# Performance work log

Hardware: AMD Instinct MI355X
Metric: run time of the kernel (lower is better)

Reference implementation:

```python
import jax, jax.numpy as jnp
import numpy as np
from jax.scipy.special import gammaln

N_TIMES = 131072
MAX_ITER = 4
DAMPING = 0.5
PREC_FLOOR = 1e-6
DEG = 20
TWO_PI = 2.0 * np.pi


def _gh_nodes(deg):
    # Nodes/weights such that sum(w * g(m + s*x)) = E_{N(m, s^2)}[g]
    xh, wh = np.polynomial.hermite.hermgauss(deg)
    x = np.sqrt(2.0) * xh
    w = wh / np.sqrt(np.pi)
    return jnp.asarray(x, jnp.float32), jnp.asarray(w, jnp.float32)


def _discretise_matern32(times, lam, sigma2):
    # dt_full = [0, diff(times)]; first step keeps the stationary prior.
    dt = jnp.concatenate([jnp.zeros((1,), times.dtype), jnp.diff(times)])
    ld = lam * dt
    e = jnp.exp(-ld)
    row0 = jnp.stack([1.0 + ld, dt], axis=-1)            # [N,2]
    row1 = jnp.stack([-(lam ** 2) * dt, 1.0 - ld], axis=-1)
    A = e[:, None, None] * jnp.stack([row0, row1], axis=-2)  # [N,2,2]
    P_inf = jnp.diag(jnp.stack([sigma2, (lam ** 2) * sigma2]))  # [2,2]
    Q = P_inf[None] - jnp.einsum('nij,jk,nlk->nil', A, P_inf, A)
    return A, Q, P_inf


def _kalman_filter(A_seq, Q_seq, P_inf, residual, mask, R_seq):
    # Scalar observation model with H = [1, 0].
    d = A_seq.shape[-1]
    def step(carry, inp):
        m, P, ll = carry
        A, Q, r, mk, R = inp
        m_pred = A @ m
        P_pred = A @ P @ A.T + Q
        v = r - m_pred[0]
        S = P_pred[0, 0] + R
        K = P_pred[:, 0] / S                      # Kalman gain [d]
        m_f = m_pred + mk * v * K
        P_f = P_pred - mk * S * jnp.outer(K, K)
        ll = ll - 0.5 * mk * (jnp.log(TWO_PI * S) + v * v / S)
        return (m_f, P_f, ll), (m_pred, P_pred, m_f, P_f)
    init = (jnp.zeros((d,), A_seq.dtype), P_inf, jnp.zeros((), A_seq.dtype))
    (_, _, log_marg), (m_pred, P_pred, m_filt, P_filt) = jax.lax.scan(
        step, init, (A_seq, Q_seq, residual, mask, R_seq))
    return m_pred, P_pred, m_filt, P_filt, log_marg


def _rts_smoother(m_pred, P_pred, m_filt, P_filt, A_seq):
    def step(carry, inp):
        ms_next, Ps_next = carry
        m_f, P_f, A_n, m_p, P_p = inp   # A_n, m_p, P_p are at step n+1
        # G = P_f A^T P_p^{-1}  (P_p symmetric)
        G = jnp.linalg.solve(P_p, A_n @ P_f).T
        ms = m_f + G @ (ms_next - m_p)
        Ps = P_f + G @ (Ps_next - P_p) @ G.T
        return (ms, Ps), (ms, Ps)
    init = (m_filt[-1], P_filt[-1])
    inputs = (m_filt[:-1], P_filt[:-1], A_seq[1:], m_pred[1:], P_pred[1:])
    _, (ms, Ps) = jax.lax.scan(step, init, inputs, reverse=True)
    m_s = jnp.concatenate([ms, m_filt[-1:]], axis=0)
    P_s = jnp.concatenate([Ps, P_filt[-1:]], axis=0)
    return m_s, P_s


def _smoothed_posterior(times, lam, sigma2, nat1, nat2):
    A, Q, P_inf = _discretise_matern32(times, lam, sigma2)
    R_seq = jnp.reciprocal(nat2)
    residual = nat1 / nat2          # prior mean is zero
    mask = jnp.ones_like(times)
    m_pred, P_pred, m_filt, P_filt, log_marg = _kalman_filter(
        A, Q, P_inf, residual, mask, R_seq)
    m_s, P_s = _rts_smoother(m_pred, P_pred, m_filt, P_filt, A)
    f_mean = m_s[:, 0]
    f_var = jnp.maximum(P_s[:, 0, 0], 1e-12)
    return f_mean, f_var, log_marg


def _log_prob(f, y):
    # Poisson likelihood with exp link, per scalar point.
    return y * f - jnp.exp(f) - gammaln(y + 1.0)


def setup_inputs() -> dict:
    key = jax.random.key(0)
    k1, k2 = jax.random.split(key)
    times = jnp.sort(jax.random.uniform(k1, (N_TIMES,), jnp.float32, 0.0, 1000.0))
    y = jax.random.randint(k2, (N_TIMES,), 0, 10, dtype=jnp.int32)
    return {
        'times': times,
        'y': y,
        'log_lengthscale': jnp.zeros((1,), jnp.float32),
        'log_variance': jnp.zeros((1,), jnp.float32),
    }


def reference(times, y, log_lengthscale, log_variance):
    y_f = y.astype(times.dtype)
    ell = jnp.exp(log_lengthscale[0])
    sigma2 = jnp.exp(log_variance[0])
    lam = jnp.sqrt(3.0) / ell
    x_nodes, w_nodes = _gh_nodes(DEG)
    N = times.shape[0]

    grad_fn = jax.vmap(jax.vmap(jax.grad(_log_prob)))           # [deg,N]
    hess_fn = jax.vmap(jax.vmap(jax.grad(jax.grad(_log_prob))))
    y_b = jnp.broadcast_to(y_f, (DEG, N))

    nat1 = jnp.zeros((N,), times.dtype)
    nat2 = jnp.full((N,), PREC_FLOOR, times.dtype)
    q_mean = jnp.zeros((N,), times.dtype)   # prior mean
    q_var = jnp.ones((N,), times.dtype)

    for _ in range(MAX_ITER):
        cav_prec = jnp.maximum(jnp.reciprocal(q_var) - nat2, PREC_FLOOR)
        cav_var = jnp.reciprocal(cav_prec)
        cav_mean = cav_var * (q_mean / q_var - nat1)
        f_grid = cav_mean[None, :] + jnp.sqrt(cav_var)[None, :] * x_nodes[:, None]
        g_avg = jnp.einsum('k,kn->n', w_nodes, grad_fn(f_grid, y_b))
        h_avg = jnp.einsum('k,kn->n', w_nodes, hess_fn(f_grid, y_b))
        new_prec = jnp.maximum(-h_avg, PREC_FLOOR)
        new_nat1 = g_avg + new_prec * cav_mean
        nat1 = (1.0 - DAMPING) * nat1 + DAMPING * new_nat1
        nat2 = jnp.maximum((1.0 - DAMPING) * nat2 + DAMPING * new_prec, PREC_FLOOR)
        q_mean, q_var, _ = _smoothed_posterior(times, lam, sigma2, nat1, nat2)

    return q_mean
```

## Files before the change

### kernel.cpp

```cpp
#include <hip/hip_runtime.h>
#include <math.h>

#define BLK   256
#define EPT   3
#define WIN   (BLK*EPT)
#define CHUNK 512
#define HALO  128
#define NW    (BLK/64)

typedef float v2f __attribute__((ext_vector_type(2)));

__device__ __forceinline__ float frcp(float x){ return __builtin_amdgcn_rcpf(x); }
__device__ __forceinline__ v2f mkv2(float x, float y){ v2f r; r.x=x; r.y=y; return r; }

struct FT { v2f A0,A1,b,C0,C1,e,J0,J1; };
struct ST { v2f E0,E1,g,L0,L1; };
struct BC { v2f b,C0,C1; };
struct GL { v2f g,L0,L1; };

template<typename T>
__device__ __forceinline__ T shflup(const T& v, int d){
  T r; const float* s=(const float*)&v; float* p=(float*)&r;
  constexpr int n = sizeof(T)/4;
  #pragma unroll
  for (int i=0;i<n;i++) p[i] = __shfl_up(s[i], (unsigned)d, 64);
  return r;
}
template<typename T>
__device__ __forceinline__ T shfldn(const T& v, int d){
  T r; const float* s=(const float*)&v; float* p=(float*)&r;
  constexpr int n = sizeof(T)/4;
  #pragma unroll
  for (int i=0;i<n;i++) p[i] = __shfl_down(s[i], (unsigned)d, 64);
  return r;
}
template<typename T>
__device__ __forceinline__ void lds_store(float (*arr)[NW], int col, const T& v){
  const float* s=(const float*)&v;
  constexpr int n = sizeof(T)/4;
  #pragma unroll
  for (int i=0;i<n;i++) arr[i][col] = s[i];
}
template<typename T>
__device__ __forceinline__ T lds_load(const float (*arr)[NW], int col){
  T r; float* p=(float*)&r;
  constexpr int n = sizeof(T)/4;
  #pragma unroll
  for (int i=0;i<n;i++) p[i] = arr[i][col];
  return r;
}

__device__ __forceinline__ FT comb_f(const FT& a, const FT& b){
  FT o;
  v2f T0 = a.C0.x*b.J0 + a.C0.y*b.J1; T0.x += 1.f;
  v2f T1 = a.C1.x*b.J0 + a.C1.y*b.J1; T1.y += 1.f;
  const float idet = frcp(T0.x*T1.y - T0.y*T1.x);
  const v2f M0 = idet * mkv2( T1.y, -T0.y);
  const v2f M1 = idet * mkv2(-T1.x,  T0.x);
  const v2f P0 = b.A0.x*M0 + b.A0.y*M1;
  const v2f P1 = b.A1.x*M0 + b.A1.y*M1;
  o.A0 = P0.x*a.A0 + P0.y*a.A1;
  o.A1 = P1.x*a.A0 + P1.y*a.A1;
  const v2f u = a.b + b.e.x*a.C0 + b.e.y*a.C1;
  o.b = mkv2(P0.x*u.x + P0.y*u.y + b.b.x,
             P1.x*u.x + P1.y*u.y + b.b.y);
  const v2f W0 = P0.x*a.C0 + P0.y*a.C1;
  const v2f W1 = P1.x*a.C0 + P1.y*a.C1;
  const float c00 = W0.x*b.A0.x + W0.y*b.A0.y + b.C0.x;
  const float c01 = W0.x*b.A1.x + W0.y*b.A1.y + b.C0.y;
  const float c11 = W1.x*b.A1.x + W1.y*b.A1.y + b.C1.y;
  o.C0 = mkv2(c00,c01); o.C1 = mkv2(c01,c11);
  const v2f v = b.e - (a.b.x*b.J0 + a.b.y*b.J1);
  const v2f Nv = v.x*M0 + v.y*M1;
  o.e = a.e + Nv.x*a.A0 + Nv.y*a.A1;
  const v2f X0 = M0.x*b.J0 + M1.x*b.J1;
  const v2f X1 = M0.y*b.J0 + M1.y*b.J1;
  const v2f Y0 = a.A0.x*X0 + a.A1.x*X1;
  const v2f Y1 = a.A0.y*X0 + a.A1.y*X1;
  const float j00 = Y0.x*a.A0.x + Y0.y*a.A1.x + a.J0.x;
  const float j01 = Y0.x*a.A0.y + Y0.y*a.A1.y + a.J0.y;
  const float j11 = Y1.x*a.A0.y + Y1.y*a.A1.y + a.J1.y;
  o.J0 = mkv2(j00,j01); o.J1 = mkv2(j01,j11);
  return o;
}

__device__ __forceinline__ BC comb_bc(const BC& a, const FT& b){
  BC o;
  v2f T0 = a.C0.x*b.J0 + a.C0.y*b.J1; T0.x += 1.f;
  v2f T1 = a.C1.x*b.J0 + a.C1.y*b.J1; T1.y += 1.f;
  const float idet = frcp(T0.x*T1.y - T0.y*T1.x);
  const v2f M0 = idet * mkv2( T1.y, -T0.y);
  const v2f M1 = idet * mkv2(-T1.x,  T0.x);
  const v2f P0 = b.A0.x*M0 + b.A0.y*M1;
  const v2f P1 = b.A1.x*M0 + b.A1.y*M1;
  const v2f u = a.b + b.e.x*a.C0 + b.e.y*a.C1;
  o.b = mkv2(P0.x*u.x + P0.y*u.y + b.b.x,
             P1.x*u.x + P1.y*u.y + b.b.y);
  const v2f W0 = P0.x*a.C0 + P0.y*a.C1;
  const v2f W1 = P1.x*a.C0 + P1.y*a.C1;
  const float c00 = W0.x*b.A0.x + W0.y*b.A0.y + b.C0.x;
  const float c01 = W0.x*b.A1.x + W0.y*b.A1.y + b.C0.y;
  const float c11 = W1.x*b.A1.x + W1.y*b.A1.y + b.C1.y;
  o.C0 = mkv2(c00,c01); o.C1 = mkv2(c01,c11);
  return o;
}

__device__ __forceinline__ ST comb_s(const ST& a, const ST& b){
  ST o;
  o.E0 = b.E0.x*a.E0 + b.E0.y*a.E1;
  o.E1 = b.E1.x*a.E0 + b.E1.y*a.E1;
  o.g = mkv2(b.E0.x*a.g.x + b.E0.y*a.g.y + b.g.x,
             b.E1.x*a.g.x + b.E1.y*a.g.y + b.g.y);
  const v2f W0 = b.E0.x*a.L0 + b.E0.y*a.L1;
  const v2f W1 = b.E1.x*a.L0 + b.E1.y*a.L1;
  const float l00 = W0.x*b.E0.x + W0.y*b.E0.y + b.L0.x;
  const float l01 = W0.x*b.E1.x + W0.y*b.E1.y + b.L0.y;
  const float l11 = W1.x*b.E1.x + W1.y*b.E1.y + b.L1.y;
  o.L0 = mkv2(l00,l01); o.L1 = mkv2(l01,l11);
  return o;
}
__device__ __forceinline__ GL comb_gl(const GL& a, const ST& b){
  GL o;
  o.g = mkv2(b.E0.x*a.g.x + b.E0.y*a.g.y + b.g.x,
             b.E1.x*a.g.x + b.E1.y*a.g.y + b.g.y);
  const v2f W0 = b.E0.x*a.L0 + b.E0.y*a.L1;
  const v2f W1 = b.E1.x*a.L0 + b.E1.y*a.L1;
  const float l00 = W0.x*b.E0.x + W0.y*b.E0.y + b.L0.x;
  const float l01 = W0.x*b.E1.x + W0.y*b.E1.y + b.L0.y;
  const float l11 = W1.x*b.E1.x + W1.y*b.E1.y + b.L1.y;
  o.L0 = mkv2(l00,l01); o.L1 = mkv2(l01,l11);
  return o;
}

__device__ __forceinline__ void compute_fq(double dt, double lam, double s2,
    v2f& F0, v2f& F1, v2f& Q0, v2f& Q1){
  const double ld = lam*dt, e = exp(-ld), e2 = e*e;
  F0 = mkv2((float)(e*(1.0+ld)), (float)(e*dt));
  F1 = mkv2((float)(-lam*lam*dt*e), (float)(e*(1.0-ld)));
  const float q00 = (float)(s2*(1.0 - e2*((1.0+ld)*(1.0+ld)+ld*ld)));
  const float q01 = (float)(2.0*s2*lam*e2*ld*ld);
  const float q11 = (float)(lam*lam*s2*(1.0 - e2*(ld*ld+(1.0-ld)*(1.0-ld))));
  Q0 = mkv2(q00,q01); Q1 = mkv2(q01,q11);
}

__device__ __forceinline__ FT build_felem(bool prior,
    const v2f F0, const v2f F1, const v2f Q0, const v2f Q1,
    float n1, float n2, float sigma2, float lam2s2)
{
  FT e;
  const float R = frcp(n2);
  const float yy = n1*R;
  if (prior){
    e.A0 = mkv2(0.f,0.f); e.A1 = mkv2(0.f,0.f);
    const float K0 = sigma2*frcp(sigma2 + R);
    e.b = mkv2(K0*yy, 0.f);
    e.C0 = mkv2(sigma2 - K0*sigma2, 0.f); e.C1 = mkv2(0.f, lam2s2);
    e.e = mkv2(0.f,0.f); e.J0 = mkv2(0.f,0.f); e.J1 = mkv2(0.f,0.f);
  } else {
    const float iS = frcp(Q0.x + R);
    const float K0 = Q0.x*iS, K1 = Q0.y*iS;
    const float om = 1.f - K0;
    e.A0 = om*F0;
    e.A1 = F1 - K1*F0;
    e.b = mkv2(K0*yy, K1*yy);
    e.C0 = om*Q0;
    e.C1 = mkv2(e.C0.y, Q1.y - K1*Q0.y);
    e.e = (yy*iS)*F0;
    e.J0 = (iS*F0.x)*F0;
    e.J1 = mkv2(e.J0.y, iS*F0.y*F0.y);
  }
  return e;
}

__device__ __forceinline__ ST build_selem(const v2f m, const v2f Pf0, const v2f Pf1,
    const v2f F0, const v2f F1, const v2f Q0, const v2f Q1)
{
  ST e;
  const v2f W0 = F0.x*Pf0 + F0.y*Pf1;
  const v2f W1 = F1.x*Pf0 + F1.y*Pf1;
  const float Pp00 = W0.x*F0.x + W0.y*F0.y + Q0.x;
  const float Pp01 = W0.x*F1.x + W0.y*F1.y + Q0.y;
  const float Pp11 = W1.x*F1.x + W1.y*F1.y + Q1.y;
  const float idet = frcp(Pp00*Pp11 - Pp01*Pp01);
  const v2f Pi0 = idet * mkv2( Pp11, -Pp01);
  const v2f Pi1 = idet * mkv2(-Pp01,  Pp00);
  e.E0 = W0.x*Pi0 + W1.x*Pi1;
  e.E1 = W0.y*Pi0 + W1.y*Pi1;
  const float mp0 = F0.x*m.x + F0.y*m.y;
  const float mp1 = F1.x*m.x + F1.y*m.y;
  e.g = mkv2(m.x - (e.E0.x*mp0 + e.E0.y*mp1),
             m.y - (e.E1.x*mp0 + e.E1.y*mp1));
  const v2f Ppr0 = mkv2(Pp00,Pp01), Ppr1 = mkv2(Pp01,Pp11);
  const v2f Z0 = e.E0.x*Ppr0 + e.E0.y*Ppr1;
  const v2f Z1 = e.E1.x*Ppr0 + e.E1.y*Ppr1;
  const float l00 = Pf0.x - (Z0.x*e.E0.x + Z0.y*e.E0.y);
  const float l01 = Pf0.y - (Z0.x*e.E1.x + Z0.y*e.E1.y);
  const float l11 = Pf1.y - (Z1.x*e.E1.x + Z1.y*e.E1.y);
  e.L0 = mkv2(l00,l01); e.L1 = mkv2(l01,l11);
  return e;
}

__global__ __launch_bounds__(BLK, 1) void fused_kernel(
    const float* __restrict__ times, const int* __restrict__ y,
    const float* __restrict__ ll, const float* __restrict__ lv,
    float* __restrict__ out, int N)
{
  __shared__ float shF[16][NW];
  __shared__ float shS[10][NW];

  const int t = threadIdx.x, b = blockIdx.x;
  const int lane = t & 63, w = t >> 6;
  const int cs = b * CHUNK;
  int ws = cs - HALO;
  if (ws < 0) ws = 0;
  if (ws > N - WIN) ws = N - WIN;
  const int g0 = ws + t * EPT;

  const double lamd    = sqrt(3.0)/exp((double)ll[0]);
  const double sigma2d = exp((double)lv[0]);
  const float sigma2 = (float)sigma2d;
  const float lam2s2 = (float)(lamd*lamd*sigma2d);

  v2f aF0[EPT+1], aF1[EPT+1], aQ0[EPT+1], aQ1[EPT+1];
  {
    const float tm1 = (g0 > 0) ? times[g0-1] : 0.f;
    const float t0 = times[g0];
    const float t1 = times[g0+1];
    const float t2 = times[g0+2];
    const float t3 = (g0+3 <= N-1) ? times[g0+3] : times[N-1];
    compute_fq((g0==0) ? 0.0 : ((double)t0-(double)tm1), lamd, sigma2d, aF0[0],aF1[0],aQ0[0],aQ1[0]);
    compute_fq((double)t1-(double)t0, lamd, sigma2d, aF0[1],aF1[1],aQ0[1],aQ1[1]);
    compute_fq((double)t2-(double)t1, lamd, sigma2d, aF0[2],aF1[2],aQ0[2],aQ1[2]);
    compute_fq((double)t3-(double)t2, lamd, sigma2d, aF0[3],aF1[3],aQ0[3],aQ1[3]);
  }
  float yf[EPT];
  yf[0] = (float)y[g0]; yf[1] = (float)y[g0+1]; yf[2] = (float)y[g0+2];

  float nat1[EPT], nat2[EPT], qm[EPT], qv[EPT];
  #pragma unroll
  for (int c=0;c<EPT;c++){ nat1[c]=0.f; nat2[c]=1e-6f; qm[c]=0.f; qv[c]=1.f; }

  const bool priorElem = (t == 0);
  const bool lastThr   = (t == BLK-1);

  for (int it=0; it<4; ++it){
    #pragma unroll
    for (int c=0;c<EPT;c++){
      const float iqv = frcp(qv[c]);
      const float cp = fmaxf(iqv - nat2[c], 1e-6f);
      const float cv = frcp(cp);
      const float cm = cv*(qm[c]*iqv - nat1[c]);
      const float Ee = __expf(cm + 0.5f*cv);
      const float np  = fmaxf(Ee, 1e-6f);
      const float nn1 = (yf[c] - Ee) + np*cm;
      nat1[c] = 0.5f*nat1[c] + 0.5f*nn1;
      nat2[c] = fmaxf(0.5f*nat2[c] + 0.5f*np, 1e-6f);
    }

    FT part0 = build_felem(priorElem, aF0[0],aF1[0],aQ0[0],aQ1[0],
                           nat1[0], nat2[0], sigma2, lam2s2);
    FT part1, part2;
    {
      const FT e1 = build_felem(false, aF0[1],aF1[1],aQ0[1],aQ1[1],
                                nat1[1], nat2[1], sigma2, lam2s2);
      part1 = comb_f(part0, e1);
      const FT e2 = build_felem(false, aF0[2],aF1[2],aQ0[2],aQ1[2],
                                nat1[2], nat2[2], sigma2, lam2s2);
      part2 = comb_f(part1, e2);
    }
    FT acc = part2;
    #pragma unroll
    for (int d=1; d<64; d<<=1){
      const FT pre_ = shflup(acc, d);
      if (lane >= d) acc = comb_f(pre_, acc);
    }
    if (lane == 63) lds_store(shF, w, acc);
    __syncthreads();
    BC pre; pre.b=mkv2(0.f,0.f); pre.C0=mkv2(0.f,0.f); pre.C1=mkv2(0.f,0.f);
    for (int j=0; j<w; ++j){
      const FT a = lds_load<FT>(shF, j);
      pre = comb_bc(pre, a);
    }
    {
      const FT lex = shflup(acc, 1);
      if (lane > 0) pre = comb_bc(pre, lex);
    }
    v2f mv[EPT], Pr0[EPT], Pr1[EPT];
    {
      const BC r0 = comb_bc(pre, part0);
      const BC r1 = comb_bc(pre, part1);
      const BC r2 = comb_bc(pre, part2);
      mv[0]=r0.b; Pr0[0]=r0.C0; Pr1[0]=r0.C1;
      mv[1]=r1.b; Pr0[1]=r1.C0; Pr1[1]=r1.C1;
      mv[2]=r2.b; Pr0[2]=r2.C0; Pr1[2]=r2.C1;
    }

    const int rw = NW-1-w;
    ST spart2;
    if (lastThr){
      spart2.E0 = mkv2(0.f,0.f); spart2.E1 = mkv2(0.f,0.f);
      spart2.g = mv[2]; spart2.L0 = Pr0[2]; spart2.L1 = Pr1[2];
    } else {
      spart2 = build_selem(mv[2], Pr0[2], Pr1[2], aF0[3],aF1[3],aQ0[3],aQ1[3]);
    }
    ST spart1, spart0;
    {
      const ST e1 = build_selem(mv[1], Pr0[1], Pr1[1], aF0[2],aF1[2],aQ0[2],aQ1[2]);
      spart1 = comb_s(spart2, e1);
      const ST e0 = build_selem(mv[0], Pr0[0], Pr1[0], aF0[1],aF1[1],aQ0[1],aQ1[1]);
      spart0 = comb_s(spart1, e0);
    }
    ST sacc = spart0;
    #pragma unroll
    for (int d=1; d<64; d<<=1){
      const ST pres = shfldn(sacc, d);
      if (lane + d < 64) sacc = comb_s(pres, sacc);
    }
    if (lane == 0) lds_store(shS, rw, sacc);
    __syncthreads();
    GL spre; spre.g=mkv2(0.f,0.f); spre.L0=mkv2(0.f,0.f); spre.L1=mkv2(0.f,0.f);
    for (int j=0; j<rw; ++j){
      const ST a = lds_load<ST>(shS, j);
      spre = comb_gl(spre, a);
    }
    {
      const ST slex = shfldn(sacc, 1);
      if (lane < 63) spre = comb_gl(spre, slex);
    }
    {
      const GL r0 = comb_gl(spre, spart0);
      const GL r1 = comb_gl(spre, spart1);
      const GL r2 = comb_gl(spre, spart2);
      qm[0] = r0.g.x; qv[0] = fmaxf(r0.L0.x, 1e-12f);
      qm[1] = r1.g.x; qv[1] = fmaxf(r1.L0.x, 1e-12f);
      qm[2] = r2.g.x; qv[2] = fmaxf(r2.L0.x, 1e-12f);
    }

    if (it == 3){
      #pragma unroll
      for (int c=0;c<EPT;c++){
        const int g = g0 + c;
        if (g >= cs && g < cs + CHUNK) out[g] = qm[c];
      }
    }
  }
}

extern "C" void kernel_launch(void* const* d_in, const int* in_sizes, int n_in,
                              void* d_out, int out_size, void* d_ws, size_t ws_size,
                              hipStream_t stream) {
  (void)n_in; (void)out_size; (void)d_ws; (void)ws_size;
  const int N = in_sizes[0];
  const float* times = (const float*)d_in[0];
  const int*   y     = (const int*)d_in[1];
  const float* ll    = (const float*)d_in[2];
  const float* lv    = (const float*)d_in[3];
  float* out = (float*)d_out;

  const int G = N / CHUNK;
  fused_kernel<<<G, BLK, 0, stream>>>(times, y, ll, lv, out, N);
}
```

Baseline: 27.67 us.

## Replace RTS backward scan with two-filter smoothing via concurrent suffix scan

```diff
diff --git a/kernel.cpp b/kernel.cpp
--- a/kernel.cpp
+++ b/kernel.cpp
@@ -14,9 +14,8 @@
 __device__ __forceinline__ v2f mkv2(float x, float y){ v2f r; r.x=x; r.y=y; return r; }
 
 struct FT { v2f A0,A1,b,C0,C1,e,J0,J1; };
-struct ST { v2f E0,E1,g,L0,L1; };
 struct BC { v2f b,C0,C1; };
-struct GL { v2f g,L0,L1; };
+struct EJ { v2f e,J0,J1; };
 
 template<typename T>
 __device__ __forceinline__ T shflup(const T& v, int d){
@@ -105,31 +104,39 @@
   return o;
 }
 
-__device__ __forceinline__ ST comb_s(const ST& a, const ST& b){
-  ST o;
-  o.E0 = b.E0.x*a.E0 + b.E0.y*a.E1;
-  o.E1 = b.E1.x*a.E0 + b.E1.y*a.E1;
-  o.g = mkv2(b.E0.x*a.g.x + b.E0.y*a.g.y + b.g.x,
-             b.E1.x*a.g.x + b.E1.y*a.g.y + b.g.y);
-  const v2f W0 = b.E0.x*a.L0 + b.E0.y*a.L1;
-  const v2f W1 = b.E1.x*a.L0 + b.E1.y*a.L1;
-  const float l00 = W0.x*b.E0.x + W0.y*b.E0.y + b.L0.x;
-  const float l01 = W0.x*b.E1.x + W0.y*b.E1.y + b.L0.y;
-  const float l11 = W1.x*b.E1.x + W1.y*b.E1.y + b.L1.y;
-  o.L0 = mkv2(l00,l01); o.L1 = mkv2(l01,l11);
+__device__ __forceinline__ EJ comb_eJ(const FT& a, const EJ& b){
+  EJ o;
+  v2f T0 = a.C0.x*b.J0 + a.C0.y*b.J1; T0.x += 1.f;
+  v2f T1 = a.C1.x*b.J0 + a.C1.y*b.J1; T1.y += 1.f;
+  const float idet = frcp(T0.x*T1.y - T0.y*T1.x);
+  const v2f M0 = idet * mkv2( T1.y, -T0.y);
+  const v2f M1 = idet * mkv2(-T1.x,  T0.x);
+  const v2f v = b.e - (a.b.x*b.J0 + a.b.y*b.J1);
+  const v2f Nv = v.x*M0 + v.y*M1;
+  o.e = a.e + Nv.x*a.A0 + Nv.y*a.A1;
+  const v2f X0 = M0.x*b.J0 + M1.x*b.J1;
+  const v2f X1 = M0.y*b.J0 + M1.y*b.J1;
+  const v2f Y0 = a.A0.x*X0 + a.A1.x*X1;
+  const v2f Y1 = a.A0.y*X0 + a.A1.y*X1;
+  const float j00 = Y0.x*a.A0.x + Y0.y*a.A1.x + a.J0.x;
+  const float j01 = Y0.x*a.A0.y + Y0.y*a.A1.y + a.J0.y;
+  const float j11 = Y1.x*a.A0.y + Y1.y*a.A1.y + a.J1.y;
+  o.J0 = mkv2(j00,j01); o.J1 = mkv2(j01,j11);
   return o;
 }
-__device__ __forceinline__ GL comb_gl(const GL& a, const ST& b){
-  GL o;
-  o.g = mkv2(b.E0.x*a.g.x + b.E0.y*a.g.y + b.g.x,
-             b.E1.x*a.g.x + b.E1.y*a.g.y + b.g.y);
-  const v2f W0 = b.E0.x*a.L0 + b.E0.y*a.L1;
-  const v2f W1 = b.E1.x*a.L0 + b.E1.y*a.L1;
-  const float l00 = W0.x*b.E0.x + W0.y*b.E0.y + b.L0.x;
-  const float l01 = W0.x*b.E1.x + W0.y*b.E1.y + b.L0.y;
-  const float l11 = W1.x*b.E1.x + W1.y*b.E1.y + b.L1.y;
-  o.L0 = mkv2(l00,l01); o.L1 = mkv2(l01,l11);
-  return o;
+
+__device__ __forceinline__ void merge_out(const v2f mf, const v2f Pf0, const v2f Pf1,
+    const EJ& s, float& oqm, float& oqv){
+  const float U00 = Pf0.x*s.J0.x + Pf0.y*s.J0.y;
+  const float U01 = Pf0.x*s.J0.y + Pf0.y*s.J1.y;
+  const float U10 = Pf1.x*s.J0.x + Pf1.y*s.J0.y;
+  const float U11 = Pf1.x*s.J0.y + Pf1.y*s.J1.y;
+  const float T00 = 1.f + U00, T01 = U01, T10 = U10, T11 = 1.f + U11;
+  const float idet = frcp(T00*T11 - T01*T10);
+  const float w0 = mf.x + Pf0.x*s.e.x + Pf0.y*s.e.y;
+  const float w1 = mf.y + Pf1.x*s.e.x + Pf1.y*s.e.y;
+  oqm = idet*(T11*w0 - T01*w1);
+  oqv = fmaxf(idet*(T11*Pf0.x - T01*Pf1.x), 1e-12f);
 }
 
 __device__ __forceinline__ void compute_fq(double dt, double lam, double s2,
@@ -172,41 +179,12 @@
   return e;
 }
 
-__device__ __forceinline__ ST build_selem(const v2f m, const v2f Pf0, const v2f Pf1,
-    const v2f F0, const v2f F1, const v2f Q0, const v2f Q1)
-{
-  ST e;
-  const v2f W0 = F0.x*Pf0 + F0.y*Pf1;
-  const v2f W1 = F1.x*Pf0 + F1.y*Pf1;
-  const float Pp00 = W0.x*F0.x + W0.y*F0.y + Q0.x;
-  const float Pp01 = W0.x*F1.x + W0.y*F1.y + Q0.y;
-  const float Pp11 = W1.x*F1.x + W1.y*F1.y + Q1.y;
-  const float idet = frcp(Pp00*Pp11 - Pp01*Pp01);
-  const v2f Pi0 = idet * mkv2( Pp11, -Pp01);
-  const v2f Pi1 = idet * mkv2(-Pp01,  Pp00);
-  e.E0 = W0.x*Pi0 + W1.x*Pi1;
-  e.E1 = W0.y*Pi0 + W1.y*Pi1;
-  const float mp0 = F0.x*m.x + F0.y*m.y;
-  const float mp1 = F1.x*m.x + F1.y*m.y;
-  e.g = mkv2(m.x - (e.E0.x*mp0 + e.E0.y*mp1),
-             m.y - (e.E1.x*mp0 + e.E1.y*mp1));
-  const v2f Ppr0 = mkv2(Pp00,Pp01), Ppr1 = mkv2(Pp01,Pp11);
-  const v2f Z0 = e.E0.x*Ppr0 + e.E0.y*Ppr1;
-  const v2f Z1 = e.E1.x*Ppr0 + e.E1.y*Ppr1;
-  const float l00 = Pf0.x - (Z0.x*e.E0.x + Z0.y*e.E0.y);
-  const float l01 = Pf0.y - (Z0.x*e.E1.x + Z0.y*e.E1.y);
-  const float l11 = Pf1.y - (Z1.x*e.E1.x + Z1.y*e.E1.y);
-  e.L0 = mkv2(l00,l01); e.L1 = mkv2(l01,l11);
-  return e;
-}
-
 __global__ __launch_bounds__(BLK, 1) void fused_kernel(
     const float* __restrict__ times, const int* __restrict__ y,
     const float* __restrict__ ll, const float* __restrict__ lv,
     float* __restrict__ out, int N)
 {
-  __shared__ float shF[16][NW];
-  __shared__ float shS[10][NW];
+  __shared__ float shF[2][16][NW];
 
   const int t = threadIdx.x, b = blockIdx.x;
   const int lane = t & 63, w = t >> 6;
@@ -221,17 +199,15 @@
   const float sigma2 = (float)sigma2d;
   const float lam2s2 = (float)(lamd*lamd*sigma2d);
 
-  v2f aF0[EPT+1], aF1[EPT+1], aQ0[EPT+1], aQ1[EPT+1];
+  v2f aF0[EPT], aF1[EPT], aQ0[EPT], aQ1[EPT];
   {
     const float tm1 = (g0 > 0) ? times[g0-1] : 0.f;
     const float t0 = times[g0];
     const float t1 = times[g0+1];
     const float t2 = times[g0+2];
-    const float t3 = (g0+3 <= N-1) ? times[g0+3] : times[N-1];
     compute_fq((g0==0) ? 0.0 : ((double)t0-(double)tm1), lamd, sigma2d, aF0[0],aF1[0],aQ0[0],aQ1[0]);
     compute_fq((double)t1-(double)t0, lamd, sigma2d, aF0[1],aF1[1],aQ0[1],aQ1[1]);
     compute_fq((double)t2-(double)t1, lamd, sigma2d, aF0[2],aF1[2],aQ0[2],aQ1[2]);
-    compute_fq((double)t3-(double)t2, lamd, sigma2d, aF0[3],aF1[3],aQ0[3],aQ1[3]);
   }
   float yf[EPT];
   yf[0] = (float)y[g0]; yf[1] = (float)y[g0+1]; yf[2] = (float)y[g0+2];
@@ -241,9 +217,10 @@
   for (int c=0;c<EPT;c++){ nat1[c]=0.f; nat2[c]=1e-6f; qm[c]=0.f; qv[c]=1.f; }
 
   const bool priorElem = (t == 0);
-  const bool lastThr   = (t == BLK-1);
 
   for (int it=0; it<4; ++it){
+    float (*shFc)[NW] = shF[it & 1];
+
     #pragma unroll
     for (int c=0;c<EPT;c++){
       const float iqv = frcp(qv[c]);
@@ -257,32 +234,35 @@
       nat2[c] = fmaxf(0.5f*nat2[c] + 0.5f*np, 1e-6f);
     }
 
-    FT part0 = build_felem(priorElem, aF0[0],aF1[0],aQ0[0],aQ1[0],
-                           nat1[0], nat2[0], sigma2, lam2s2);
-    FT part1, part2;
-    {
-      const FT e1 = build_felem(false, aF0[1],aF1[1],aQ0[1],aQ1[1],
-                                nat1[1], nat2[1], sigma2, lam2s2);
-      part1 = comb_f(part0, e1);
-      const FT e2 = build_felem(false, aF0[2],aF1[2],aQ0[2],aQ1[2],
-                                nat1[2], nat2[2], sigma2, lam2s2);
-      part2 = comb_f(part1, e2);
-    }
-    FT acc = part2;
+    const FT part0 = build_felem(priorElem, aF0[0],aF1[0],aQ0[0],aQ1[0],
+                                 nat1[0], nat2[0], sigma2, lam2s2);
+    const FT e1 = build_felem(false, aF0[1],aF1[1],aQ0[1],aQ1[1],
+                              nat1[1], nat2[1], sigma2, lam2s2);
+    const FT part1 = comb_f(part0, e1);
+    const FT e2 = build_felem(false, aF0[2],aF1[2],aQ0[2],aQ1[2],
+                              nat1[2], nat2[2], sigma2, lam2s2);
+    const FT part2 = comb_f(part1, e2);
+
+    FT facc = part2;
+    FT sacc = part2;
     #pragma unroll
     for (int d=1; d<64; d<<=1){
-      const FT pre_ = shflup(acc, d);
-      if (lane >= d) acc = comb_f(pre_, acc);
-    }
-    if (lane == 63) lds_store(shF, w, acc);
+      const FT fpre = shflup(facc, d);
+      const FT snxt = shfldn(sacc, d);
+      if (lane >= d)     facc = comb_f(fpre, facc);
+      if (lane + d < 64) sacc = comb_f(sacc, snxt);
+    }
+    if (lane == 63) lds_store(shFc, w, facc);
+    const FT Sl1 = shfldn(sacc, 1);
     __syncthreads();
+
     BC pre; pre.b=mkv2(0.f,0.f); pre.C0=mkv2(0.f,0.f); pre.C1=mkv2(0.f,0.f);
     for (int j=0; j<w; ++j){
-      const FT a = lds_load<FT>(shF, j);
+      const FT a = lds_load<FT>(shFc, j);
       pre = comb_bc(pre, a);
     }
     {
-      const FT lex = shflup(acc, 1);
+      const FT lex = shflup(facc, 1);
       if (lane > 0) pre = comb_bc(pre, lex);
     }
     v2f mv[EPT], Pr0[EPT], Pr1[EPT];
@@ -295,46 +275,18 @@
       mv[2]=r2.b; Pr0[2]=r2.C0; Pr1[2]=r2.C1;
     }
 
-    const int rw = NW-1-w;
-    ST spart2;
-    if (lastThr){
-      spart2.E0 = mkv2(0.f,0.f); spart2.E1 = mkv2(0.f,0.f);
-      spart2.g = mv[2]; spart2.L0 = Pr0[2]; spart2.L1 = Pr1[2];
-    } else {
-      spart2 = build_selem(mv[2], Pr0[2], Pr1[2], aF0[3],aF1[3],aQ0[3],aQ1[3]);
-    }
-    ST spart1, spart0;
-    {
-      const ST e1 = build_selem(mv[1], Pr0[1], Pr1[1], aF0[2],aF1[2],aQ0[2],aQ1[2]);
-      spart1 = comb_s(spart2, e1);
-      const ST e0 = build_selem(mv[0], Pr0[0], Pr1[0], aF0[1],aF1[1],aQ0[1],aQ1[1]);
-      spart0 = comb_s(spart1, e0);
-    }
-    ST sacc = spart0;
-    #pragma unroll
-    for (int d=1; d<64; d<<=1){
-      const ST pres = shfldn(sacc, d);
-      if (lane + d < 64) sacc = comb_s(pres, sacc);
-    }
-    if (lane == 0) lds_store(shS, rw, sacc);
-    __syncthreads();
-    GL spre; spre.g=mkv2(0.f,0.f); spre.L0=mkv2(0.f,0.f); spre.L1=mkv2(0.f,0.f);
-    for (int j=0; j<rw; ++j){
-      const ST a = lds_load<ST>(shS, j);
-      spre = comb_gl(spre, a);
-    }
-    {
-      const ST slex = shfldn(sacc, 1);
-      if (lane < 63) spre = comb_gl(spre, slex);
-    }
-    {
-      const GL r0 = comb_gl(spre, spart0);
-      const GL r1 = comb_gl(spre, spart1);
-      const GL r2 = comb_gl(spre, spart2);
-      qm[0] = r0.g.x; qv[0] = fmaxf(r0.L0.x, 1e-12f);
-      qm[1] = r1.g.x; qv[1] = fmaxf(r1.L0.x, 1e-12f);
-      qm[2] = r2.g.x; qv[2] = fmaxf(r2.L0.x, 1e-12f);
-    }
+    EJ cr; cr.e=mkv2(0.f,0.f); cr.J0=mkv2(0.f,0.f); cr.J1=mkv2(0.f,0.f);
+    for (int j=NW-1; j>w; --j){
+      const FT a = lds_load<FT>(shFc, j);
+      cr = comb_eJ(a, cr);
+    }
+    if (lane < 63) cr = comb_eJ(Sl1, cr);
+    const EJ suf2 = cr;
+    const EJ suf1 = comb_eJ(e2, suf2);
+    const EJ suf0 = comb_eJ(e1, suf1);
+    merge_out(mv[0], Pr0[0], Pr1[0], suf0, qm[0], qv[0]);
+    merge_out(mv[1], Pr0[1], Pr1[1], suf1, qm[1], qv[1]);
+    merge_out(mv[2], Pr0[2], Pr1[2], suf2, qm[2], qv[2]);
 
     if (it == 3){
       #pragma unroll
```

Measured after the change: 30.98 us. 12.0% more time.
